# Kernel optimization log

Measured on AMD Instinct MI355X. Metric: run time of the kernel, lower is better.

The kernel has to match this reference:

```python
import jax, jax.numpy as jnp
import numpy as np

USER_NUM = 100000
ITEM_NUM = 100000
N_NODES = USER_NUM + ITEM_NUM
N_EDGES = 4000000
EMB = 64
N_LAYERS = 3


def setup_inputs() -> dict:
    key = jax.random.key(0)
    k1, k2, k3, k4, k5 = jax.random.split(key, 5)
    user_emb = jax.random.normal(k1, (USER_NUM, EMB), dtype=jnp.float32) * 0.1
    item_emb = jax.random.normal(k2, (ITEM_NUM, EMB), dtype=jnp.float32) * 0.1
    adj_row = jax.random.randint(k3, (N_EDGES,), 0, N_NODES, dtype=jnp.int32)
    adj_col = jax.random.randint(k4, (N_EDGES,), 0, N_NODES, dtype=jnp.int32)
    # normalized-laplacian-like positive edge weights
    adj_val = jax.random.uniform(k5, (N_EDGES,), dtype=jnp.float32) * 0.05
    return {"user_emb": user_emb, "item_emb": item_emb,
            "adj_row": adj_row, "adj_col": adj_col, "adj_val": adj_val}


def _spmm(row, col, val, x):
    # sparse [N,N] @ dense [N,d] via gather + segment-sum over destination rows
    msgs = val[:, None] * x[col]              # [E, d]
    return jax.ops.segment_sum(msgs, row, num_segments=N_NODES)


def reference(user_emb, item_emb, adj_row, adj_col, adj_val):
    ego = jnp.concatenate([user_emb, item_emb], axis=0)  # [N, d]
    acc = ego                                            # running sum over layers
    for _ in range(N_LAYERS):
        ego = _spmm(adj_row, adj_col, adj_val, ego)
        acc = acc + ego
    all_emb = acc / jnp.float32(N_LAYERS + 1)            # mean over n_layers+1 embeddings
    return all_emb[:USER_NUM], all_emb[USER_NUM:]
```

## Files before the change

kernel.cpp:

```cpp
#include <hip/hip_runtime.h>
#include <stdint.h>


constexpr int N_USER = 100000;
constexpr int NN     = 200000;
constexpr int NE     = 4000000;
constexpr int EMB    = 64;

__global__ __launch_bounds__(256) void init_kernel(
    const float4* __restrict__ user, const float4* __restrict__ item,
    float4* __restrict__ A, float4* __restrict__ acc)
{
    const int64_t half  = (int64_t)N_USER * EMB / 4;
    const int64_t total = (int64_t)NN * EMB / 4;
    for (int64_t i = blockIdx.x * (int64_t)blockDim.x + threadIdx.x; i < total;
         i += (int64_t)gridDim.x * blockDim.x) {
        const float4 v = (i < half) ? user[i] : item[i - half];
        A[i] = v;
        acc[i] = v;
    }
}

__global__ __launch_bounds__(256) void hist_kernel(
    const int* __restrict__ rows, int* __restrict__ cnt)
{
    for (int e = blockIdx.x * blockDim.x + threadIdx.x; e < NE;
         e += gridDim.x * blockDim.x)
        atomicAdd(&cnt[rows[e]], 1);
}

__global__ __launch_bounds__(1024) void scan_kernel(
    const int* __restrict__ cnt, int* __restrict__ rowptr)
{
    __shared__ int sums[1024];
    const int t  = threadIdx.x;
    const int CH = (NN + 1023) / 1024;
    const int start = t * CH;
    const int end   = (start + CH < NN) ? start + CH : NN;

    int s = 0;
    for (int i = start; i < end; ++i) s += cnt[i];
    sums[t] = s;
    __syncthreads();

    for (int off = 1; off < 1024; off <<= 1) {
        const int x = sums[t];
        const int y = (t >= off) ? sums[t - off] : 0;
        __syncthreads();
        sums[t] = x + y;
        __syncthreads();
    }

    int run = (t == 0) ? 0 : sums[t - 1];
    for (int i = start; i < end; ++i) {
        rowptr[i] = run;
        run += cnt[i];
    }
    if (t == 0) rowptr[NN] = sums[1023];
}

__global__ __launch_bounds__(256) void scatter_kernel(
    const int* __restrict__ rows, const int* __restrict__ cols,
    const int* __restrict__ vals_bits, int* __restrict__ cursor,
    int2* __restrict__ csr_cv)
{
    for (int e = blockIdx.x * blockDim.x + threadIdx.x; e < NE;
         e += gridDim.x * blockDim.x) {
        const int r = rows[e];
        const int p = atomicAdd(&cursor[r], 1);
        csr_cv[p] = make_int2(cols[e], vals_bits[e]);
    }
}

__global__ __launch_bounds__(256) void spmm_csr_kernel(
    const int* __restrict__ rowptr, const int2* __restrict__ csr_cv,
    const float* __restrict__ x, float* __restrict__ y)
{
    const int lane = threadIdx.x & 63;
    const int wave = (int)((blockIdx.x * (int64_t)blockDim.x + threadIdx.x) >> 6);
    const int nw   = (int)(((int64_t)gridDim.x * blockDim.x) >> 6);

    for (int r = wave; r < NN; r += nw) {
        const int e0 = rowptr[r];
        const int e1 = rowptr[r + 1];
        float acc = 0.f;
        #pragma unroll 4
        for (int e = e0; e < e1; ++e) {
            const int2  cv = csr_cv[e];
            const float v  = __builtin_bit_cast(float, cv.y);
            acc = fmaf(v, x[(int64_t)cv.x * EMB + lane], acc);
        }
        y[(int64_t)r * EMB + lane] = acc;
    }
}

__global__ __launch_bounds__(256) void acc_add_kernel(
    float4* __restrict__ acc, const float4* __restrict__ y)
{
    const int64_t total = (int64_t)NN * EMB / 4;
    for (int64_t i = blockIdx.x * (int64_t)blockDim.x + threadIdx.x; i < total;
         i += (int64_t)gridDim.x * blockDim.x) {
        float4 a = acc[i];
        const float4 b = y[i];
        a.x += b.x; a.y += b.y; a.z += b.z; a.w += b.w;
        acc[i] = a;
    }
}

__global__ __launch_bounds__(256) void acc_final_kernel(
    float4* __restrict__ acc, const float4* __restrict__ y)
{
    const int64_t total = (int64_t)NN * EMB / 4;
    for (int64_t i = blockIdx.x * (int64_t)blockDim.x + threadIdx.x; i < total;
         i += (int64_t)gridDim.x * blockDim.x) {
        float4 a = acc[i];
        const float4 b = y[i];
        a.x = (a.x + b.x) * 0.25f;
        a.y = (a.y + b.y) * 0.25f;
        a.z = (a.z + b.z) * 0.25f;
        a.w = (a.w + b.w) * 0.25f;
        acc[i] = a;
    }
}

extern "C" void kernel_launch(void* const* d_in, const int* in_sizes, int n_in,
                              void* d_out, int out_size, void* d_ws, size_t ws_size,
                              hipStream_t stream)
{
    const float* user = (const float*)d_in[0];
    const float* item = (const float*)d_in[1];
    const int*   rows = (const int*)d_in[2];
    const int*   cols = (const int*)d_in[3];
    const int*   vals = (const int*)d_in[4];

    float* acc = (float*)d_out;

    char* ws = (char*)d_ws;
    const size_t VEC_B = (size_t)NN * EMB * sizeof(float);
    const size_t RP_B  = ((size_t)(NN + 1) * 4 + 255) & ~255ull;
    const size_t CC_B  = ((size_t)NN * 4 + 255) & ~255ull;
    float* A      = (float*)(ws);
    float* B      = (float*)(ws + VEC_B);
    int*   rowptr = (int*)  (ws + 2 * VEC_B);
    int*   cntcur = (int*)  (ws + 2 * VEC_B + RP_B);
    int2*  csr_cv = (int2*) (ws + 2 * VEC_B + RP_B + CC_B);

    const dim3 blk(256);
    const int eltBlocks  = 1024;
    const int edgeBlocks = 2048;
    const int spmmBlocks = 4096;

    init_kernel<<<eltBlocks, blk, 0, stream>>>(
        (const float4*)user, (const float4*)item, (float4*)A, (float4*)acc);
    hipMemsetAsync(cntcur, 0, (size_t)NN * 4, stream);
    hist_kernel<<<edgeBlocks, blk, 0, stream>>>(rows, cntcur);
    scan_kernel<<<1, 1024, 0, stream>>>(cntcur, rowptr);
    hipMemcpyAsync(cntcur, rowptr, (size_t)NN * 4, hipMemcpyDeviceToDevice, stream);
    scatter_kernel<<<edgeBlocks, blk, 0, stream>>>(rows, cols, vals, cntcur, csr_cv);

    spmm_csr_kernel<<<spmmBlocks, blk, 0, stream>>>(rowptr, csr_cv, A, B);
    acc_add_kernel<<<eltBlocks, blk, 0, stream>>>((float4*)acc, (const float4*)B);

    spmm_csr_kernel<<<spmmBlocks, blk, 0, stream>>>(rowptr, csr_cv, B, A);
    acc_add_kernel<<<eltBlocks, blk, 0, stream>>>((float4*)acc, (const float4*)A);

    spmm_csr_kernel<<<spmmBlocks, blk, 0, stream>>>(rowptr, csr_cv, A, B);
    acc_final_kernel<<<eltBlocks, blk, 0, stream>>>((float4*)acc, (const float4*)B);
}
```

Measured before the change: 1.454 ms.

## Two-level bucketed CSR build, fused accumulation, and float4 edge-parallel SpMM

CSR construction now runs in two passes. Edges are first binned into 64-row buckets, with the local row packed into the column bits, and then each bucket is sorted by row in shared memory. This cuts global atomic contention and the scattered writes of the per-row scatter. The layer accumulation is fused into the SpMM kernels, which removes the separate acc_add/acc_final passes. The first and last layers use a float4 layout where four edge groups per wave are reduced with shuffles. The bcv buffer aliases B, which is safe only because B is first written after the CSR build. Packing assumes column indices fit in 18 bits.

```diff
diff --git a/kernel.cpp b/kernel.cpp
--- a/kernel.cpp
+++ b/kernel.cpp
@@ -6,43 +6,47 @@
 constexpr int NN     = 200000;
 constexpr int NE     = 4000000;
 constexpr int EMB    = 64;
+constexpr int RPB    = 64;
+constexpr int NB     = NN / RPB;
+constexpr int COLB   = 18;
 
 __global__ __launch_bounds__(256) void init_kernel(
     const float4* __restrict__ user, const float4* __restrict__ item,
-    float4* __restrict__ A, float4* __restrict__ acc)
+    float4* __restrict__ A, float4* __restrict__ acc, int* __restrict__ bhist)
 {
     const int64_t half  = (int64_t)N_USER * EMB / 4;
     const int64_t total = (int64_t)NN * EMB / 4;
-    for (int64_t i = blockIdx.x * (int64_t)blockDim.x + threadIdx.x; i < total;
-         i += (int64_t)gridDim.x * blockDim.x) {
+    const int64_t tid0  = blockIdx.x * (int64_t)blockDim.x + threadIdx.x;
+    for (int64_t i = tid0; i < total; i += (int64_t)gridDim.x * blockDim.x) {
         const float4 v = (i < half) ? user[i] : item[i - half];
         A[i] = v;
         acc[i] = v;
     }
-}
-
-__global__ __launch_bounds__(256) void hist_kernel(
-    const int* __restrict__ rows, int* __restrict__ cnt)
+    if (tid0 < NB) bhist[tid0] = 0;
+}
+
+__global__ __launch_bounds__(256) void bhist_kernel(
+    const int* __restrict__ rows, int* __restrict__ bhist)
 {
     for (int e = blockIdx.x * blockDim.x + threadIdx.x; e < NE;
          e += gridDim.x * blockDim.x)
-        atomicAdd(&cnt[rows[e]], 1);
-}
-
-__global__ __launch_bounds__(1024) void scan_kernel(
-    const int* __restrict__ cnt, int* __restrict__ rowptr)
+        atomicAdd(&bhist[rows[e] >> 6], 1);
+}
+
+__global__ __launch_bounds__(1024) void bscan_kernel(
+    const int* __restrict__ bhist, int* __restrict__ bucketBase,
+    int* __restrict__ bcursor, int* __restrict__ rowptr)
 {
     __shared__ int sums[1024];
     const int t  = threadIdx.x;
-    const int CH = (NN + 1023) / 1024;
+    const int CH = (NB + 1023) / 1024;
     const int start = t * CH;
-    const int end   = (start + CH < NN) ? start + CH : NN;
+    const int end   = (start + CH < NB) ? start + CH : NB;
 
     int s = 0;
-    for (int i = start; i < end; ++i) s += cnt[i];
+    for (int i = start; i < end; ++i) s += bhist[i];
     sums[t] = s;
     __syncthreads();
-
     for (int off = 1; off < 1024; off <<= 1) {
         const int x = sums[t];
         const int y = (t >= off) ? sums[t - off] : 0;
@@ -50,31 +54,150 @@
         sums[t] = x + y;
         __syncthreads();
     }
-
     int run = (t == 0) ? 0 : sums[t - 1];
     for (int i = start; i < end; ++i) {
-        rowptr[i] = run;
-        run += cnt[i];
-    }
-    if (t == 0) rowptr[NN] = sums[1023];
-}
-
-__global__ __launch_bounds__(256) void scatter_kernel(
+        bucketBase[i] = run;
+        bcursor[i] = 0;
+        run += bhist[i];
+    }
+    if (t == 0) { bucketBase[NB] = NE; rowptr[NN] = NE; }
+}
+
+__global__ __launch_bounds__(256) void bin_kernel(
     const int* __restrict__ rows, const int* __restrict__ cols,
-    const int* __restrict__ vals_bits, int* __restrict__ cursor,
-    int2* __restrict__ csr_cv)
+    const int* __restrict__ vals_bits, const int* __restrict__ bucketBase,
+    int* __restrict__ bcursor, int2* __restrict__ bcv)
 {
     for (int e = blockIdx.x * blockDim.x + threadIdx.x; e < NE;
          e += gridDim.x * blockDim.x) {
         const int r = rows[e];
-        const int p = atomicAdd(&cursor[r], 1);
-        csr_cv[p] = make_int2(cols[e], vals_bits[e]);
-    }
-}
-
-__global__ __launch_bounds__(256) void spmm_csr_kernel(
-    const int* __restrict__ rowptr, const int2* __restrict__ csr_cv,
-    const float* __restrict__ x, float* __restrict__ y)
+        const int b = r >> 6;
+        const int p = bucketBase[b] + atomicAdd(&bcursor[b], 1);
+        bcv[p] = make_int2(((r & 63) << COLB) | cols[e], vals_bits[e]);
+    }
+}
+
+__global__ __launch_bounds__(256) void bucket_csr_kernel(
+    const int* __restrict__ bucketBase, const int2* __restrict__ bcv,
+    int2* __restrict__ csr_cv, int* __restrict__ rowptr)
+{
+    __shared__ int lcnt[RPB];
+    __shared__ int lcur[RPB];
+    const int b    = blockIdx.x;
+    const int t    = threadIdx.x;
+    const int base = bucketBase[b];
+    const int cnt  = bucketBase[b + 1] - base;
+
+    if (t < RPB) lcnt[t] = 0;
+    __syncthreads();
+    for (int i = t; i < cnt; i += 256)
+        atomicAdd(&lcnt[((unsigned)bcv[base + i].x) >> COLB], 1);
+    __syncthreads();
+    if (t < 64) {
+        const int v = lcnt[t];
+        int s = v;
+        #pragma unroll
+        for (int off = 1; off < 64; off <<= 1) {
+            const int u = __shfl_up(s, off, 64);
+            if (t >= off) s += u;
+        }
+        const int excl = s - v;
+        lcur[t] = excl;
+        rowptr[b * RPB + t] = base + excl;
+    }
+    __syncthreads();
+    for (int i = t; i < cnt; i += 256) {
+        const int2 pv = bcv[base + i];
+        const int  lr = ((unsigned)pv.x) >> COLB;
+        const int  p  = atomicAdd(&lcur[lr], 1);
+        csr_cv[base + p] = make_int2(pv.x & ((1 << COLB) - 1), pv.y);
+    }
+}
+
+__device__ __forceinline__ float4 spmm_row_wide(
+    const int* __restrict__ rowptr, const int2* __restrict__ csr_cv,
+    const float4* __restrict__ x4, int r, int g, int sub)
+{
+    const int e0 = rowptr[r];
+    const int e1 = rowptr[r + 1];
+    float4 s0 = make_float4(0.f, 0.f, 0.f, 0.f);
+    float4 s1 = make_float4(0.f, 0.f, 0.f, 0.f);
+    int e = e0 + g;
+    for (; e + 4 < e1; e += 8) {
+        const int2 cv0 = csr_cv[e];
+        const int2 cv1 = csr_cv[e + 4];
+        const float4 x0 = x4[(int64_t)cv0.x * (EMB / 4) + sub];
+        const float4 x1 = x4[(int64_t)cv1.x * (EMB / 4) + sub];
+        const float v0 = __builtin_bit_cast(float, cv0.y);
+        const float v1 = __builtin_bit_cast(float, cv1.y);
+        s0.x = fmaf(v0, x0.x, s0.x); s0.y = fmaf(v0, x0.y, s0.y);
+        s0.z = fmaf(v0, x0.z, s0.z); s0.w = fmaf(v0, x0.w, s0.w);
+        s1.x = fmaf(v1, x1.x, s1.x); s1.y = fmaf(v1, x1.y, s1.y);
+        s1.z = fmaf(v1, x1.z, s1.z); s1.w = fmaf(v1, x1.w, s1.w);
+    }
+    if (e < e1) {
+        const int2 cv = csr_cv[e];
+        const float4 xv = x4[(int64_t)cv.x * (EMB / 4) + sub];
+        const float v = __builtin_bit_cast(float, cv.y);
+        s0.x = fmaf(v, xv.x, s0.x); s0.y = fmaf(v, xv.y, s0.y);
+        s0.z = fmaf(v, xv.z, s0.z); s0.w = fmaf(v, xv.w, s0.w);
+    }
+    float4 s = make_float4(s0.x + s1.x, s0.y + s1.y, s0.z + s1.z, s0.w + s1.w);
+    s.x += __shfl_xor(s.x, 16, 64); s.y += __shfl_xor(s.y, 16, 64);
+    s.z += __shfl_xor(s.z, 16, 64); s.w += __shfl_xor(s.w, 16, 64);
+    s.x += __shfl_xor(s.x, 32, 64); s.y += __shfl_xor(s.y, 32, 64);
+    s.z += __shfl_xor(s.z, 32, 64); s.w += __shfl_xor(s.w, 32, 64);
+    return s;
+}
+
+__global__ __launch_bounds__(256) void spmm_wide_kernel(
+    const int* __restrict__ rowptr, const int2* __restrict__ csr_cv,
+    const float4* __restrict__ x4, float4* __restrict__ y4,
+    float4* __restrict__ acc4)
+{
+    const int lane = threadIdx.x & 63;
+    const int g    = lane >> 4;
+    const int sub  = lane & 15;
+    const int wave = (int)((blockIdx.x * (int64_t)blockDim.x + threadIdx.x) >> 6);
+    const int nw   = (int)(((int64_t)gridDim.x * blockDim.x) >> 6);
+
+    for (int r = wave; r < NN; r += nw) {
+        const float4 s = spmm_row_wide(rowptr, csr_cv, x4, r, g, sub);
+        if (g == 0) {
+            const int64_t idx = (int64_t)r * (EMB / 4) + sub;
+            y4[idx] = s;
+            float4 a = acc4[idx];
+            a.x += s.x; a.y += s.y; a.z += s.z; a.w += s.w;
+            acc4[idx] = a;
+        }
+    }
+}
+
+__global__ __launch_bounds__(256) void spmm_final_wide_kernel(
+    const int* __restrict__ rowptr, const int2* __restrict__ csr_cv,
+    const float4* __restrict__ x4, float4* __restrict__ acc4)
+{
+    const int lane = threadIdx.x & 63;
+    const int g    = lane >> 4;
+    const int sub  = lane & 15;
+    const int wave = (int)((blockIdx.x * (int64_t)blockDim.x + threadIdx.x) >> 6);
+    const int nw   = (int)(((int64_t)gridDim.x * blockDim.x) >> 6);
+
+    for (int r = wave; r < NN; r += nw) {
+        const float4 s = spmm_row_wide(rowptr, csr_cv, x4, r, g, sub);
+        if (g == 0) {
+            const int64_t idx = (int64_t)r * (EMB / 4) + sub;
+            float4 a = acc4[idx];
+            a.x = (a.x + s.x) * 0.25f; a.y = (a.y + s.y) * 0.25f;
+            a.z = (a.z + s.z) * 0.25f; a.w = (a.w + s.w) * 0.25f;
+            acc4[idx] = a;
+        }
+    }
+}
+
+__global__ __launch_bounds__(256) void spmm_simple_kernel(
+    const int* __restrict__ rowptr, const int2* __restrict__ csr_cv,
+    const float* __restrict__ x, float* __restrict__ y, float* __restrict__ acc)
 {
     const int lane = threadIdx.x & 63;
     const int wave = (int)((blockIdx.x * (int64_t)blockDim.x + threadIdx.x) >> 6);
@@ -83,43 +206,26 @@
     for (int r = wave; r < NN; r += nw) {
         const int e0 = rowptr[r];
         const int e1 = rowptr[r + 1];
-        float acc = 0.f;
-        #pragma unroll 4
-        for (int e = e0; e < e1; ++e) {
-            const int2  cv = csr_cv[e];
-            const float v  = __builtin_bit_cast(float, cv.y);
-            acc = fmaf(v, x[(int64_t)cv.x * EMB + lane], acc);
-        }
-        y[(int64_t)r * EMB + lane] = acc;
-    }
-}
-
-__global__ __launch_bounds__(256) void acc_add_kernel(
-    float4* __restrict__ acc, const float4* __restrict__ y)
-{
-    const int64_t total = (int64_t)NN * EMB / 4;
-    for (int64_t i = blockIdx.x * (int64_t)blockDim.x + threadIdx.x; i < total;
-         i += (int64_t)gridDim.x * blockDim.x) {
-        float4 a = acc[i];
-        const float4 b = y[i];
-        a.x += b.x; a.y += b.y; a.z += b.z; a.w += b.w;
-        acc[i] = a;
-    }
-}
-
-__global__ __launch_bounds__(256) void acc_final_kernel(
-    float4* __restrict__ acc, const float4* __restrict__ y)
-{
-    const int64_t total = (int64_t)NN * EMB / 4;
-    for (int64_t i = blockIdx.x * (int64_t)blockDim.x + threadIdx.x; i < total;
-         i += (int64_t)gridDim.x * blockDim.x) {
-        float4 a = acc[i];
-        const float4 b = y[i];
-        a.x = (a.x + b.x) * 0.25f;
-        a.y = (a.y + b.y) * 0.25f;
-        a.z = (a.z + b.z) * 0.25f;
-        a.w = (a.w + b.w) * 0.25f;
-        acc[i] = a;
+        float s0 = 0.f, s1 = 0.f;
+        int e = e0;
+        #pragma unroll 2
+        for (; e + 1 < e1; e += 2) {
+            const int2 cv0 = csr_cv[e];
+            const int2 cv1 = csr_cv[e + 1];
+            s0 = fmaf(__builtin_bit_cast(float, cv0.y),
+                      x[(int64_t)cv0.x * EMB + lane], s0);
+            s1 = fmaf(__builtin_bit_cast(float, cv1.y),
+                      x[(int64_t)cv1.x * EMB + lane], s1);
+        }
+        if (e < e1) {
+            const int2 cv = csr_cv[e];
+            s0 = fmaf(__builtin_bit_cast(float, cv.y),
+                      x[(int64_t)cv.x * EMB + lane], s0);
+        }
+        const float s = s0 + s1;
+        const int64_t idx = (int64_t)r * EMB + lane;
+        y[idx] = s;
+        acc[idx] += s;
     }
 }
 
@@ -137,33 +243,34 @@
 
     char* ws = (char*)d_ws;
     const size_t VEC_B = (size_t)NN * EMB * sizeof(float);
-    const size_t RP_B  = ((size_t)(NN + 1) * 4 + 255) & ~255ull;
-    const size_t CC_B  = ((size_t)NN * 4 + 255) & ~255ull;
     float* A      = (float*)(ws);
     float* B      = (float*)(ws + VEC_B);
-    int*   rowptr = (int*)  (ws + 2 * VEC_B);
-    int*   cntcur = (int*)  (ws + 2 * VEC_B + RP_B);
-    int2*  csr_cv = (int2*) (ws + 2 * VEC_B + RP_B + CC_B);
+    int2*  bcv    = (int2*) (ws + VEC_B);
+    char*  tail   = ws + 2 * VEC_B;
+    int*   rowptr = (int*)(tail);                    tail += ((size_t)(NN + 1) * 4 + 255) & ~255ull;
+    int*   bucketBase = (int*)(tail);                tail += ((size_t)(NB + 1) * 4 + 255) & ~255ull;
+    int*   bhist  = (int*)(tail);                    tail += ((size_t)NB * 4 + 255) & ~255ull;
+    int*   bcursor= (int*)(tail);                    tail += ((size_t)NB * 4 + 255) & ~255ull;
+    int2*  csr_cv = (int2*)(tail);
 
     const dim3 blk(256);
-    const int eltBlocks  = 1024;
-    const int edgeBlocks = 2048;
-    const int spmmBlocks = 4096;
+    const int eltBlocks   = 1024;
+    const int edgeBlocks  = 2048;
+    const int wideBlocks  = 12500;
+    const int simpBlocks  = 4096;
 
     init_kernel<<<eltBlocks, blk, 0, stream>>>(
-        (const float4*)user, (const float4*)item, (float4*)A, (float4*)acc);
-    hipMemsetAsync(cntcur, 0, (size_t)NN * 4, stream);
-    hist_kernel<<<edgeBlocks, blk, 0, stream>>>(rows, cntcur);
-    scan_kernel<<<1, 1024, 0, stream>>>(cntcur, rowptr);
-    hipMemcpyAsync(cntcur, rowptr, (size_t)NN * 4, hipMemcpyDeviceToDevice, stream);
-    scatter_kernel<<<edgeBlocks, blk, 0, stream>>>(rows, cols, vals, cntcur, csr_cv);
-
-    spmm_csr_kernel<<<spmmBlocks, blk, 0, stream>>>(rowptr, csr_cv, A, B);
-    acc_add_kernel<<<eltBlocks, blk, 0, stream>>>((float4*)acc, (const float4*)B);
-
-    spmm_csr_kernel<<<spmmBlocks, blk, 0, stream>>>(rowptr, csr_cv, B, A);
-    acc_add_kernel<<<eltBlocks, blk, 0, stream>>>((float4*)acc, (const float4*)A);
-
-    spmm_csr_kernel<<<spmmBlocks, blk, 0, stream>>>(rowptr, csr_cv, A, B);
-    acc_final_kernel<<<eltBlocks, blk, 0, stream>>>((float4*)acc, (const float4*)B);
-}
+        (const float4*)user, (const float4*)item, (float4*)A, (float4*)acc, bhist);
+    bhist_kernel<<<edgeBlocks, blk, 0, stream>>>(rows, bhist);
+    bscan_kernel<<<1, 1024, 0, stream>>>(bhist, bucketBase, bcursor, rowptr);
+    bin_kernel<<<edgeBlocks, blk, 0, stream>>>(rows, cols, vals, bucketBase,
+                                               bcursor, bcv);
+    bucket_csr_kernel<<<NB, blk, 0, stream>>>(bucketBase, bcv, csr_cv, rowptr);
+
+    spmm_wide_kernel<<<wideBlocks, blk, 0, stream>>>(rowptr, csr_cv,
+        (const float4*)A, (float4*)B, (float4*)acc);
+    spmm_simple_kernel<<<simpBlocks, blk, 0, stream>>>(rowptr, csr_cv,
+        B, A, acc);
+    spmm_final_wide_kernel<<<wideBlocks, blk, 0, stream>>>(rowptr, csr_cv,
+        (const float4*)A, (float4*)acc);
+}
```

New measurement: 1.310 ms. 9.9% less time.

## Replace per-row CSR build with 64-row bucket binning and shared-memory SpMM

Applied to the files above, without the earlier changes.

Edges are now binned into buckets of 64 destination rows using per-workgroup LDS histograms, a single scan, and LDS-cursor scatter. This removes the global per-row atomics and the memset and device-to-device copy of the old CSR build. The SpMM processes one bucket per block, accumulating into an LDS tile with shared-memory atomics, and fuses the layer-sum and final scaling into the writeback, so the separate accumulate kernels are gone. The cost is an LDS atomic per edge per lane, load imbalance across buckets, and an 18-bit column packing limit; ghist aliases buffer B, which is safe because it is consumed before B is written.

```diff
diff --git a/kernel.cpp b/kernel.cpp
--- a/kernel.cpp
+++ b/kernel.cpp
@@ -6,6 +6,13 @@
 constexpr int NN     = 200000;
 constexpr int NE     = 4000000;
 constexpr int EMB    = 64;
+constexpr int RPB    = 64;
+constexpr int NB     = NN / RPB;
+constexpr int COLB   = 18;
+constexpr int CMASK  = (1 << COLB) - 1;
+constexpr int NWG    = 128;
+constexpr int EPW    = NE / NWG;
+constexpr int SCN    = NB * NWG;
 
 __global__ __launch_bounds__(256) void init_kernel(
     const float4* __restrict__ user, const float4* __restrict__ item,
@@ -21,28 +28,34 @@
     }
 }
 
-__global__ __launch_bounds__(256) void hist_kernel(
-    const int* __restrict__ rows, int* __restrict__ cnt)
+__global__ __launch_bounds__(1024) void ghist_kernel(
+    const int* __restrict__ rows, int* __restrict__ ghist)
 {
-    for (int e = blockIdx.x * blockDim.x + threadIdx.x; e < NE;
-         e += gridDim.x * blockDim.x)
-        atomicAdd(&cnt[rows[e]], 1);
+    __shared__ int lh[NB];
+    const int g = blockIdx.x, t = threadIdx.x;
+    for (int i = t; i < NB; i += 1024) lh[i] = 0;
+    __syncthreads();
+    const int lo = g * EPW, hi = lo + EPW;
+    for (int e = lo + t; e < hi; e += 1024)
+        atomicAdd(&lh[rows[e] >> 6], 1);
+    __syncthreads();
+    for (int i = t; i < NB; i += 1024)
+        ghist[(int64_t)i * NWG + g] = lh[i];
 }
 
 __global__ __launch_bounds__(1024) void scan_kernel(
-    const int* __restrict__ cnt, int* __restrict__ rowptr)
+    int* __restrict__ gh, int* __restrict__ bucketBase)
 {
     __shared__ int sums[1024];
-    const int t  = threadIdx.x;
-    const int CH = (NN + 1023) / 1024;
+    const int t = threadIdx.x;
+    constexpr int CH = (SCN + 1023) / 1024;
     const int start = t * CH;
-    const int end   = (start + CH < NN) ? start + CH : NN;
+    const int end   = (start + CH < SCN) ? start + CH : SCN;
 
     int s = 0;
-    for (int i = start; i < end; ++i) s += cnt[i];
+    for (int i = start; i < end; ++i) s += gh[i];
     sums[t] = s;
     __syncthreads();
-
     for (int off = 1; off < 1024; off <<= 1) {
         const int x = sums[t];
         const int y = (t >= off) ? sums[t - off] : 0;
@@ -50,76 +63,89 @@
         sums[t] = x + y;
         __syncthreads();
     }
-
     int run = (t == 0) ? 0 : sums[t - 1];
     for (int i = start; i < end; ++i) {
-        rowptr[i] = run;
-        run += cnt[i];
+        const int v = gh[i];
+        gh[i] = run;
+        if ((i & (NWG - 1)) == 0) bucketBase[i / NWG] = run;
+        run += v;
     }
-    if (t == 0) rowptr[NN] = sums[1023];
+    if (t == 0) bucketBase[NB] = NE;
 }
 
-__global__ __launch_bounds__(256) void scatter_kernel(
+__global__ __launch_bounds__(1024) void bin_kernel(
     const int* __restrict__ rows, const int* __restrict__ cols,
-    const int* __restrict__ vals_bits, int* __restrict__ cursor,
-    int2* __restrict__ csr_cv)
+    const int* __restrict__ vals_bits, const int* __restrict__ base,
+    int2* __restrict__ bcv)
 {
-    for (int e = blockIdx.x * blockDim.x + threadIdx.x; e < NE;
-         e += gridDim.x * blockDim.x) {
+    __shared__ int lcur[NB];
+    const int g = blockIdx.x, t = threadIdx.x;
+    for (int i = t; i < NB; i += 1024)
+        lcur[i] = base[(int64_t)i * NWG + g];
+    __syncthreads();
+    const int lo = g * EPW, hi = lo + EPW;
+    for (int e = lo + t; e < hi; e += 1024) {
         const int r = rows[e];
-        const int p = atomicAdd(&cursor[r], 1);
-        csr_cv[p] = make_int2(cols[e], vals_bits[e]);
+        const int p = atomicAdd(&lcur[r >> 6], 1);
+        bcv[p] = make_int2(((r & 63) << COLB) | cols[e], vals_bits[e]);
     }
 }
 
-__global__ __launch_bounds__(256) void spmm_csr_kernel(
-    const int* __restrict__ rowptr, const int2* __restrict__ csr_cv,
-    const float* __restrict__ x, float* __restrict__ y)
+template<bool FINAL>
+__global__ __launch_bounds__(256) void spmm_bucket_kernel(
+    const int* __restrict__ bucketBase, const int2* __restrict__ bcv,
+    const float* __restrict__ x, float4* __restrict__ y4,
+    float4* __restrict__ acc4)
 {
-    const int lane = threadIdx.x & 63;
-    const int wave = (int)((blockIdx.x * (int64_t)blockDim.x + threadIdx.x) >> 6);
-    const int nw   = (int)(((int64_t)gridDim.x * blockDim.x) >> 6);
+    __shared__ float tile[RPB * EMB];
+    float4* t4 = (float4*)tile;
+    const int b = blockIdx.x, t = threadIdx.x;
+    for (int i = t; i < RPB * EMB / 4; i += 256)
+        t4[i] = make_float4(0.f, 0.f, 0.f, 0.f);
+    __syncthreads();
 
-    for (int r = wave; r < NN; r += nw) {
-        const int e0 = rowptr[r];
-        const int e1 = rowptr[r + 1];
-        float acc = 0.f;
-        #pragma unroll 4
-        for (int e = e0; e < e1; ++e) {
-            const int2  cv = csr_cv[e];
-            const float v  = __builtin_bit_cast(float, cv.y);
-            acc = fmaf(v, x[(int64_t)cv.x * EMB + lane], acc);
+    const int lane = t & 63, wv = t >> 6;
+    const int e0 = bucketBase[b], e1 = bucketBase[b + 1];
+    int e = e0 + wv;
+    for (; e + 12 < e1; e += 16) {
+        const int2 c0 = bcv[e];
+        const int2 c1 = bcv[e + 4];
+        const int2 c2 = bcv[e + 8];
+        const int2 c3 = bcv[e + 12];
+        const float x0 = x[(int64_t)(c0.x & CMASK) * EMB + lane];
+        const float x1 = x[(int64_t)(c1.x & CMASK) * EMB + lane];
+        const float x2 = x[(int64_t)(c2.x & CMASK) * EMB + lane];
+        const float x3 = x[(int64_t)(c3.x & CMASK) * EMB + lane];
+        atomicAdd(&tile[(((unsigned)c0.x) >> COLB) * EMB + lane],
+                  __builtin_bit_cast(float, c0.y) * x0);
+        atomicAdd(&tile[(((unsigned)c1.x) >> COLB) * EMB + lane],
+                  __builtin_bit_cast(float, c1.y) * x1);
+        atomicAdd(&tile[(((unsigned)c2.x) >> COLB) * EMB + lane],
+                  __builtin_bit_cast(float, c2.y) * x2);
+        atomicAdd(&tile[(((unsigned)c3.x) >> COLB) * EMB + lane],
+                  __builtin_bit_cast(float, c3.y) * x3);
+    }
+    for (; e < e1; e += 4) {
+        const int2 c = bcv[e];
+        const float xv = x[(int64_t)(c.x & CMASK) * EMB + lane];
+        atomicAdd(&tile[(((unsigned)c.x) >> COLB) * EMB + lane],
+                  __builtin_bit_cast(float, c.y) * xv);
+    }
+    __syncthreads();
+
+    for (int i = t; i < RPB * EMB / 4; i += 256) {
+        const float4 s = t4[i];
+        const int64_t idx = (int64_t)b * (RPB * EMB / 4) + i;
+        float4 a = acc4[idx];
+        if constexpr (FINAL) {
+            a.x = (a.x + s.x) * 0.25f; a.y = (a.y + s.y) * 0.25f;
+            a.z = (a.z + s.z) * 0.25f; a.w = (a.w + s.w) * 0.25f;
+            acc4[idx] = a;
+        } else {
+            y4[idx] = s;
+            a.x += s.x; a.y += s.y; a.z += s.z; a.w += s.w;
+            acc4[idx] = a;
         }
-        y[(int64_t)r * EMB + lane] = acc;
-    }
-}
-
-__global__ __launch_bounds__(256) void acc_add_kernel(
-    float4* __restrict__ acc, const float4* __restrict__ y)
-{
-    const int64_t total = (int64_t)NN * EMB / 4;
-    for (int64_t i = blockIdx.x * (int64_t)blockDim.x + threadIdx.x; i < total;
-         i += (int64_t)gridDim.x * blockDim.x) {
-        float4 a = acc[i];
-        const float4 b = y[i];
-        a.x += b.x; a.y += b.y; a.z += b.z; a.w += b.w;
-        acc[i] = a;
-    }
-}
-
-__global__ __launch_bounds__(256) void acc_final_kernel(
-    float4* __restrict__ acc, const float4* __restrict__ y)
-{
-    const int64_t total = (int64_t)NN * EMB / 4;
-    for (int64_t i = blockIdx.x * (int64_t)blockDim.x + threadIdx.x; i < total;
-         i += (int64_t)gridDim.x * blockDim.x) {
-        float4 a = acc[i];
-        const float4 b = y[i];
-        a.x = (a.x + b.x) * 0.25f;
-        a.y = (a.y + b.y) * 0.25f;
-        a.z = (a.z + b.z) * 0.25f;
-        a.w = (a.w + b.w) * 0.25f;
-        acc[i] = a;
     }
 }
 
@@ -137,33 +163,25 @@
 
     char* ws = (char*)d_ws;
     const size_t VEC_B = (size_t)NN * EMB * sizeof(float);
-    const size_t RP_B  = ((size_t)(NN + 1) * 4 + 255) & ~255ull;
-    const size_t CC_B  = ((size_t)NN * 4 + 255) & ~255ull;
-    float* A      = (float*)(ws);
-    float* B      = (float*)(ws + VEC_B);
-    int*   rowptr = (int*)  (ws + 2 * VEC_B);
-    int*   cntcur = (int*)  (ws + 2 * VEC_B + RP_B);
-    int2*  csr_cv = (int2*) (ws + 2 * VEC_B + RP_B + CC_B);
+    float* A     = (float*)(ws);
+    float* B     = (float*)(ws + VEC_B);
+    int*   ghist = (int*)  (ws + VEC_B);
+    int2*  bcv   = (int2*) (ws + 2 * VEC_B);
+    int*   bucketBase = (int*)(ws + 2 * VEC_B + (size_t)NE * sizeof(int2));
 
-    const dim3 blk(256);
-    const int eltBlocks  = 1024;
-    const int edgeBlocks = 2048;
-    const int spmmBlocks = 4096;
+    const dim3 blk256(256), blk1k(1024);
+    const int eltBlocks = 1024;
 
-    init_kernel<<<eltBlocks, blk, 0, stream>>>(
+    init_kernel<<<eltBlocks, blk256, 0, stream>>>(
         (const float4*)user, (const float4*)item, (float4*)A, (float4*)acc);
-    hipMemsetAsync(cntcur, 0, (size_t)NN * 4, stream);
-    hist_kernel<<<edgeBlocks, blk, 0, stream>>>(rows, cntcur);
-    scan_kernel<<<1, 1024, 0, stream>>>(cntcur, rowptr);
-    hipMemcpyAsync(cntcur, rowptr, (size_t)NN * 4, hipMemcpyDeviceToDevice, stream);
-    scatter_kernel<<<edgeBlocks, blk, 0, stream>>>(rows, cols, vals, cntcur, csr_cv);
+    ghist_kernel<<<NWG, blk1k, 0, stream>>>(rows, ghist);
+    scan_kernel<<<1, blk1k, 0, stream>>>(ghist, bucketBase);
+    bin_kernel<<<NWG, blk1k, 0, stream>>>(rows, cols, vals, ghist, bcv);
 
-    spmm_csr_kernel<<<spmmBlocks, blk, 0, stream>>>(rowptr, csr_cv, A, B);
-    acc_add_kernel<<<eltBlocks, blk, 0, stream>>>((float4*)acc, (const float4*)B);
-
-    spmm_csr_kernel<<<spmmBlocks, blk, 0, stream>>>(rowptr, csr_cv, B, A);
-    acc_add_kernel<<<eltBlocks, blk, 0, stream>>>((float4*)acc, (const float4*)A);
-
-    spmm_csr_kernel<<<spmmBlocks, blk, 0, stream>>>(rowptr, csr_cv, A, B);
-    acc_final_kernel<<<eltBlocks, blk, 0, stream>>>((float4*)acc, (const float4*)B);
+    spmm_bucket_kernel<false><<<NB, blk256, 0, stream>>>(bucketBase, bcv,
+        A, (float4*)B, (float4*)acc);
+    spmm_bucket_kernel<false><<<NB, blk256, 0, stream>>>(bucketBase, bcv,
+        B, (float4*)A, (float4*)acc);
+    spmm_bucket_kernel<true><<<NB, blk256, 0, stream>>>(bucketBase, bcv,
+        A, (float4*)nullptr, (float4*)acc);
 }
```

Measured after the change: 5.044 ms. +246.8%, slower.
